# Kernel optimization log

Hardware: AMD Instinct MI355X
Metric: run time of the kernel (lower is better)

The kernel has to match this reference:

```python
import jax, jax.numpy as jnp
import numpy as np

GRID = 32          # grid_size -> N = 1024 patches
NPT = 1            # num_prefix_tokens
SCALE = 8.0        # sqrt(dim_head=64)
EPS = 1e-5         # nn.LayerNorm default eps


def _ln(x, g, b):
    m = jnp.mean(x, axis=-1, keepdims=True)
    v = jnp.var(x, axis=-1, keepdims=True)
    return (x - m) / jnp.sqrt(v + EPS) * g + b


def setup_inputs() -> dict:
    key = jax.random.key(0)
    ks = jax.random.split(key, 12)
    B, T, D, Dh = 32, GRID * GRID + NPT, 768, 64
    s = 0.02
    return {
        "x": jax.random.normal(ks[0], (B, T, D), jnp.float32),
        "Wq": jax.random.normal(ks[1], (D, Dh), jnp.float32) * s,
        "Wk": jax.random.normal(ks[2], (D, Dh), jnp.float32) * s,
        "Wv": jax.random.normal(ks[3], (D, Dh), jnp.float32) * s,
        "gq": jnp.ones((Dh,), jnp.float32),
        "bq": jnp.zeros((Dh,), jnp.float32),
        "gk": jnp.ones((Dh,), jnp.float32),
        "bk": jnp.zeros((Dh,), jnp.float32),
        "Wsig": jax.random.normal(ks[4], (Dh, 2), jnp.float32) * s,
        "bsig": jnp.zeros((2,), jnp.float32),
        "Wa": jax.random.normal(ks[5], (Dh, 1), jnp.float32) * s,
        "ba": jnp.zeros((1,), jnp.float32),
    }


def reference(x, Wq, Wk, Wv, gq, bq, gk, bk, Wsig, bsig, Wa, ba):
    # x: [B, T, D] with T = GRID^2 + NPT
    q = _ln(x @ Wq, gq, bq)            # [B, T, Dh]
    k = _ln(x @ Wk, gk, bk)            # [B, T, Dh]
    v = x @ Wv                          # [B, T, Dh]

    q_patch = q[:, NPT:, :]             # [B, N, Dh]
    alpha = jax.nn.softplus(q_patch @ Wa + ba)[..., 0]   # [B, N]
    sig = jax.nn.sigmoid(q_patch @ Wsig + bsig)          # [B, N, 2]
    sx, sy = sig[..., 0], sig[..., 1]                     # [B, N] each

    # patch-grid relative displacements (vectorized replacement of the
    # O(N^2) python double loop)
    ii, jj = jnp.meshgrid(jnp.arange(GRID), jnp.arange(GRID), indexing="ij")
    coords = jnp.stack([ii.ravel(), jj.ravel()], axis=-1).astype(jnp.float32)  # [N,2]=(y,x)
    dy = coords[:, None, 0] - coords[None, :, 0]          # [N, N]
    dx = coords[:, None, 1] - coords[None, :, 1]          # [N, N]

    # Gaussian bias: G[b,p,q] = exp(-dx^2/(2 sx[b,p]^2) - dy^2/(2 sy[b,p]^2))
    G = jnp.exp(-(dx * dx) / (2.0 * sx[:, :, None] ** 2)
                - (dy * dy) / (2.0 * sy[:, :, None] ** 2))  # [B, N, N]
    S = alpha[:, :, None] * G                               # [B, N, N]

    sim = jnp.einsum("bqd,bkd->bqk", q, k)                  # [B, T, T]
    sim = sim.at[:, NPT:, NPT:].add(S)

    probs = jax.nn.softmax(sim / SCALE, axis=-1)
    return probs @ v                                         # [B, T, Dh]
```

## Files before the change

kernel.cpp:

```cpp
#include <hip/hip_runtime.h>
#include <hip/hip_bf16.h>
#include <math.h>

#define BDIM 32
#define TDIM 1025
#define DDIM 768
#define GRIDW 32
#define TPATCH 1024
#define SCALE 8.0f
#define EPSLN 1e-5f
#define NROW (BDIM * TDIM)
#define VTLD 1088
#define LDP  72
#define LDQ  40
#define NTILES 17

typedef __attribute__((ext_vector_type(8))) short short8v;
typedef __attribute__((ext_vector_type(4))) float f32x4;

__device__ __forceinline__ unsigned short f2bf(float f) {
    unsigned int u = __float_as_uint(f);
    u += 0x7FFFu + ((u >> 16) & 1u);
    return (unsigned short)(u >> 16);
}

__device__ __forceinline__ short8v pack8(float4 a, float4 b) {
    union { short8v v; unsigned short s[8]; } u;
    u.s[0] = f2bf(a.x); u.s[1] = f2bf(a.y); u.s[2] = f2bf(a.z); u.s[3] = f2bf(a.w);
    u.s[4] = f2bf(b.x); u.s[5] = f2bf(b.y); u.s[6] = f2bf(b.z); u.s[7] = f2bf(b.w);
    return u.v;
}

__device__ __forceinline__ void wg_barrier() {
    asm volatile("s_waitcnt lgkmcnt(0)" ::: "memory");
    __builtin_amdgcn_s_barrier();
    __builtin_amdgcn_sched_barrier(0);
}

template<int CTRL>
__device__ __forceinline__ float dpp_f(float x) {
    return __int_as_float(__builtin_amdgcn_update_dpp(
        __float_as_int(x), __float_as_int(x), CTRL, 0xF, 0xF, true));
}
__device__ __forceinline__ float red16_max(float x) {
    x = fmaxf(x, dpp_f<0xB1>(x));
    x = fmaxf(x, dpp_f<0x4E>(x));
    x = fmaxf(x, dpp_f<0x124>(x));
    x = fmaxf(x, dpp_f<0x128>(x));
    return x;
}
__device__ __forceinline__ float red16_sum(float x) {
    x += dpp_f<0xB1>(x);
    x += dpp_f<0x4E>(x);
    x += dpp_f<0x124>(x);
    x += dpp_f<0x128>(x);
    return x;
}

__global__ __launch_bounds__(256) void prep_w_kernel(
    const float* __restrict__ Wq, const float* __restrict__ Wk,
    const float* __restrict__ Wv, unsigned short* __restrict__ wT)
{
    const int c = blockIdx.x;
    const float* W = (c < 64) ? Wq : (c < 128) ? Wk : Wv;
    const int cc = c & 63;
    for (int k = threadIdx.x; k < DDIM; k += 256)
        wT[(size_t)c * DDIM + k] = f2bf(W[(size_t)k * 64 + cc]);
}

__global__ __launch_bounds__(256) void qkv_tile_kernel(
    const float* __restrict__ x, const unsigned short* __restrict__ wT,
    const float* __restrict__ gq, const float* __restrict__ bq,
    const float* __restrict__ gk, const float* __restrict__ bk,
    const float* __restrict__ Wsig, const float* __restrict__ bsig,
    const float* __restrict__ Wa, const float* __restrict__ ba,
    unsigned short* __restrict__ qb, unsigned short* __restrict__ kb,
    unsigned short* __restrict__ vb,
    float* __restrict__ a8, float* __restrict__ isx, float* __restrict__ isy)
{
    __shared__ unsigned short As[2][64][LDQ];
    __shared__ unsigned short Bs[2][192][LDQ];

    const int t  = threadIdx.x;
    const int wv = t >> 6;
    const int ln = t & 63;
    const int lq = ln >> 4;
    const int lr = ln & 15;
    const int tok0 = blockIdx.x * 64;

    const int arow = t >> 2;
    const int aseg = t & 3;
    const float* aptr = x + (size_t)min(tok0 + arow, NROW - 1) * DDIM + aseg * 8;
    const int brow = t >> 2;
    const int bseg = t & 3;

    f32x4 acc[12];
#pragma unroll
    for (int ni = 0; ni < 12; ++ni) acc[ni] = (f32x4){0.f, 0.f, 0.f, 0.f};

    float4 ra0, ra1;
    short8v rb0, rb1, rb2;

    ra0 = *(const float4*)(aptr + 0);
    ra1 = *(const float4*)(aptr + 4);
    rb0 = *(const short8v*)&wT[(size_t)(brow +   0) * DDIM + bseg * 8];
    rb1 = *(const short8v*)&wT[(size_t)(brow +  64) * DDIM + bseg * 8];
    rb2 = *(const short8v*)&wT[(size_t)(brow + 128) * DDIM + bseg * 8];

#pragma unroll
    for (int ks = 0; ks < 24; ++ks) {
        const int buf = ks & 1;
        *(short8v*)&As[buf][arow][aseg * 8]        = pack8(ra0, ra1);
        *(short8v*)&Bs[buf][brow +   0][bseg * 8]  = rb0;
        *(short8v*)&Bs[buf][brow +  64][bseg * 8]  = rb1;
        *(short8v*)&Bs[buf][brow + 128][bseg * 8]  = rb2;
        if (ks + 1 < 24) {
            const int k0 = (ks + 1) * 32;
            ra0 = *(const float4*)(aptr + k0 + 0);
            ra1 = *(const float4*)(aptr + k0 + 4);
            rb0 = *(const short8v*)&wT[(size_t)(brow +   0) * DDIM + k0 + bseg * 8];
            rb1 = *(const short8v*)&wT[(size_t)(brow +  64) * DDIM + k0 + bseg * 8];
            rb2 = *(const short8v*)&wT[(size_t)(brow + 128) * DDIM + k0 + bseg * 8];
        }
        __syncthreads();
        short8v af = *(const short8v*)&As[buf][wv * 16 + lr][lq * 8];
#pragma unroll
        for (int ni = 0; ni < 12; ++ni) {
            short8v bf = *(const short8v*)&Bs[buf][16 * ni + lr][lq * 8];
            acc[ni] = __builtin_amdgcn_mfma_f32_16x16x32_bf16(af, bf, acc[ni], 0, 0, 0);
        }
    }

    float gqv[4], bqv[4], gkv[4], bkv[4], wav[4], ws0[4], ws1[4];
#pragma unroll
    for (int ni = 0; ni < 4; ++ni) {
        int c = lr + 16 * ni;
        gqv[ni] = gq[c]; bqv[ni] = bq[c];
        gkv[ni] = gk[c]; bkv[ni] = bk[c];
        wav[ni] = Wa[c];
        ws0[ni] = Wsig[2 * c];
        ws1[ni] = Wsig[2 * c + 1];
    }
    const float ba0 = ba[0], bs0 = bsig[0], bs1 = bsig[1];

#pragma unroll
    for (int reg = 0; reg < 4; ++reg) {
        const int tokr = tok0 + wv * 16 + lq * 4 + reg;

        float s1 = 0.f, s2 = 0.f;
#pragma unroll
        for (int ni = 0; ni < 4; ++ni) {
            float v = acc[ni][reg];
            s1 += v; s2 += v * v;
        }
#pragma unroll
        for (int off = 1; off < 16; off <<= 1) {
            s1 += __shfl_xor(s1, off);
            s2 += __shfl_xor(s2, off);
        }
        float mean = s1 * (1.f / 64.f);
        float var  = s2 * (1.f / 64.f) - mean * mean;
        float rstd = rsqrtf(var + EPSLN);
        float qn[4];
#pragma unroll
        for (int ni = 0; ni < 4; ++ni)
            qn[ni] = (acc[ni][reg] - mean) * rstd * gqv[ni] + bqv[ni];

        s1 = 0.f; s2 = 0.f;
#pragma unroll
        for (int ni = 0; ni < 4; ++ni) {
            float v = acc[4 + ni][reg];
            s1 += v; s2 += v * v;
        }
#pragma unroll
        for (int off = 1; off < 16; off <<= 1) {
            s1 += __shfl_xor(s1, off);
            s2 += __shfl_xor(s2, off);
        }
        mean = s1 * (1.f / 64.f);
        var  = s2 * (1.f / 64.f) - mean * mean;
        rstd = rsqrtf(var + EPSLN);
        float kn[4];
#pragma unroll
        for (int ni = 0; ni < 4; ++ni)
            kn[ni] = (acc[4 + ni][reg] - mean) * rstd * gkv[ni] + bkv[ni];

        float da = 0.f, d0 = 0.f, d1 = 0.f;
#pragma unroll
        for (int ni = 0; ni < 4; ++ni) {
            da += qn[ni] * wav[ni];
            d0 += qn[ni] * ws0[ni];
            d1 += qn[ni] * ws1[ni];
        }
#pragma unroll
        for (int off = 1; off < 16; off <<= 1) {
            da += __shfl_xor(da, off);
            d0 += __shfl_xor(d0, off);
            d1 += __shfl_xor(d1, off);
        }

        if (tokr < NROW) {
            size_t base = (size_t)tokr * 64;
            int bidx = tokr / TDIM;
            int ti   = tokr - bidx * TDIM;
#pragma unroll
            for (int ni = 0; ni < 4; ++ni) {
                int c = lr + 16 * ni;
                qb[base + c] = f2bf(qn[ni]);
                kb[base + c] = f2bf(kn[ni]);
                vb[base + c] = f2bf(acc[8 + ni][reg]);
            }
            if (lr == 0 && ti >= 1) {
                int p = bidx * TPATCH + ti - 1;
                float av = da + ba0;
                float sp = (av > 20.f) ? av : log1pf(__expf(av));
                a8[p] = sp * (1.f / SCALE);
                float sx = 1.f / (1.f + __expf(-(d0 + bs0)));
                float sy = 1.f / (1.f + __expf(-(d1 + bs1)));
                isx[p] = 0.5f / (sx * sx);
                isy[p] = 0.5f / (sy * sy);
            }
        }
    }
}

__global__ __launch_bounds__(256) void vtrans_kernel(
    const unsigned short* __restrict__ vb, unsigned short* __restrict__ vT)
{
    __shared__ unsigned short tile[64][LDP];
    const int t  = threadIdx.x;
    const int bb = blockIdx.y;
    const int t0 = blockIdx.x * 64;

#pragma unroll
    for (int it = 0; it < 2; ++it) {
        int lin = t + it * 256;
        int tok = lin >> 3;
        int d0  = (lin & 7) * 8;
        short8v v8 = {0, 0, 0, 0, 0, 0, 0, 0};
        if (t0 + tok < TDIM)
            v8 = *(const short8v*)&vb[((size_t)bb * TDIM + t0 + tok) * 64 + d0];
        union { short8v v; unsigned short s[8]; } u; u.v = v8;
#pragma unroll
        for (int j = 0; j < 8; ++j) tile[d0 + j][tok] = u.s[j];
    }
    __syncthreads();

    const int dh = t >> 2;
    const int ch = t & 3;
    short8v o0 = *(const short8v*)&tile[dh][ch * 16];
    short8v o1 = *(const short8v*)&tile[dh][ch * 16 + 8];
    size_t dst = ((size_t)bb * 64 + dh) * VTLD + t0 + ch * 16;
    *(short8v*)&vT[dst]     = o0;
    *(short8v*)&vT[dst + 8] = o1;
}

__global__ __launch_bounds__(256) void attn_mfma_kernel(
    const unsigned short* __restrict__ qb, const unsigned short* __restrict__ kb,
    const unsigned short* __restrict__ vT,
    const float* __restrict__ a8, const float* __restrict__ isx,
    const float* __restrict__ isy, float* __restrict__ out)
{
    __shared__ unsigned short Ks[2][64][LDP];
    __shared__ unsigned short Vt[2][64][LDP];
    __shared__ unsigned short Pt[4][16][LDP];

    const int t  = threadIdx.x;
    const int wv = t >> 6;
    const int ln = t & 63;
    const int lq = ln >> 4;
    const int lr = ln & 15;
    const int bb = blockIdx.y;
    const int q0 = blockIdx.x * 64;

    const int qrow = min(q0 + wv * 16 + lr, TDIM - 1);
    const size_t qbase = ((size_t)bb * TDIM + qrow) * 64;
    const short8v aq0 = *(const short8v*)&qb[qbase + lq * 8];
    const short8v aq1 = *(const short8v*)&qb[qbase + 32 + lq * 8];

    float a8q[4], sxq[4], syq[4], qpy[4], qpx[4];
    bool  hasS[4];
#pragma unroll
    for (int reg = 0; reg < 4; ++reg) {
        int qg = q0 + wv * 16 + lq * 4 + reg;
        hasS[reg] = false;
        a8q[reg] = 0.f; sxq[reg] = 0.f; syq[reg] = 0.f; qpy[reg] = 0.f; qpx[reg] = 0.f;
        if (qg >= 1 && qg < TDIM) {
            int qp = qg - 1;
            hasS[reg] = true;
            a8q[reg] = a8 [bb * TPATCH + qp];
            sxq[reg] = isx[bb * TPATCH + qp];
            syq[reg] = isy[bb * TPATCH + qp];
            qpy[reg] = (float)(qp >> 5);
            qpx[reg] = (float)(qp & 31);
        }
    }

    float m[4]  = {-1e30f, -1e30f, -1e30f, -1e30f};
    float l[4]  = {0.f, 0.f, 0.f, 0.f};
    f32x4 oacc[4];
#pragma unroll
    for (int ni = 0; ni < 4; ++ni) oacc[ni] = (f32x4){0.f, 0.f, 0.f, 0.f};

    const int sk_row = t >> 3;
    const int sk_d0  = (t & 7) * 8;
    short8v rk[2], rv[2];

#define ALOAD(KT0)                                                             \
    do {                                                                       \
        _Pragma("unroll") for (int it = 0; it < 2; ++it) {                     \
            int key = sk_row + 32 * it;                                        \
            int kg  = (KT0) + key;                                             \
            rk[it] = (kg < TDIM)                                               \
                ? *(const short8v*)&kb[((size_t)bb * TDIM + kg) * 64 + sk_d0]  \
                : (short8v){0, 0, 0, 0, 0, 0, 0, 0};                           \
            rv[it] = *(const short8v*)&vT[((size_t)bb * 64 + key) * VTLD +     \
                                          (KT0) + sk_d0];                      \
        }                                                                      \
    } while (0)

#define ASTORE(BUF)                                                            \
    do {                                                                       \
        _Pragma("unroll") for (int it = 0; it < 2; ++it) {                     \
            *(short8v*)&Ks[BUF][sk_row + 32 * it][sk_d0] = rk[it];             \
            *(short8v*)&Vt[BUF][sk_row + 32 * it][sk_d0] = rv[it];             \
        }                                                                      \
    } while (0)

    ALOAD(0);
    ASTORE(0);
    wg_barrier();

    for (int tile = 0; tile < NTILES; ++tile) {
        const int kt0 = tile * 64;
        const int buf = tile & 1;
        if (tile + 1 < NTILES) ALOAD(kt0 + 64);

        f32x4 sac[4];
#pragma unroll
        for (int ni = 0; ni < 4; ++ni) sac[ni] = (f32x4){0.f, 0.f, 0.f, 0.f};
#pragma unroll
        for (int ni = 0; ni < 4; ++ni) {
            short8v b0 = *(const short8v*)&Ks[buf][16 * ni + lr][lq * 8];
            short8v b1 = *(const short8v*)&Ks[buf][16 * ni + lr][32 + lq * 8];
            sac[ni] = __builtin_amdgcn_mfma_f32_16x16x32_bf16(aq0, b0, sac[ni], 0, 0, 0);
            sac[ni] = __builtin_amdgcn_mfma_f32_16x16x32_bf16(aq1, b1, sac[ni], 0, 0, 0);
        }

#pragma unroll
        for (int ni = 0; ni < 4; ++ni) {
            int key = kt0 + 16 * ni + lr;
            int kp  = key - 1;
            float ky = (float)(kp >> 5);
            float kx = (float)(kp & 31);
            bool kvalid = (key >= 1) && (key < TDIM);
#pragma unroll
            for (int reg = 0; reg < 4; ++reg) {
                float z = sac[ni][reg] * (1.f / SCALE);
                if (kvalid && hasS[reg]) {
                    float dy = qpy[reg] - ky;
                    float dx = qpx[reg] - kx;
                    z += a8q[reg] * __expf(-(dx * dx * sxq[reg] + dy * dy * syq[reg]));
                }
                if (key >= TDIM) z = -1e30f;
                sac[ni][reg] = z;
            }
        }

        float scf[4];
#pragma unroll
        for (int reg = 0; reg < 4; ++reg) {
            float mx = fmaxf(fmaxf(sac[0][reg], sac[1][reg]),
                             fmaxf(sac[2][reg], sac[3][reg]));
            mx = red16_max(mx);
            float mn = fmaxf(m[reg], mx);
            scf[reg] = __expf(m[reg] - mn);
            m[reg] = mn;
            float ts = 0.f;
#pragma unroll
            for (int ni = 0; ni < 4; ++ni) {
                float pp = __expf(sac[ni][reg] - mn);
                sac[ni][reg] = pp;
                ts += pp;
            }
            ts = red16_sum(ts);
            l[reg] = l[reg] * scf[reg] + ts;
        }
#pragma unroll
        for (int ni = 0; ni < 4; ++ni)
#pragma unroll
            for (int reg = 0; reg < 4; ++reg)
                oacc[ni][reg] *= scf[reg];

#pragma unroll
        for (int ni = 0; ni < 4; ++ni)
#pragma unroll
            for (int reg = 0; reg < 4; ++reg)
                Pt[wv][lq * 4 + reg][16 * ni + lr] = f2bf(sac[ni][reg]);

#pragma unroll
        for (int ks = 0; ks < 2; ++ks) {
            short8v pa = *(const short8v*)&Pt[wv][lr][ks * 32 + lq * 8];
#pragma unroll
            for (int ni = 0; ni < 4; ++ni) {
                short8v bv = *(const short8v*)&Vt[buf][16 * ni + lr][ks * 32 + lq * 8];
                oacc[ni] = __builtin_amdgcn_mfma_f32_16x16x32_bf16(pa, bv, oacc[ni], 0, 0, 0);
            }
        }

        if (tile + 1 < NTILES) ASTORE(buf ^ 1);
        wg_barrier();
    }
#undef ALOAD
#undef ASTORE

#pragma unroll
    for (int reg = 0; reg < 4; ++reg) {
        int qg = q0 + wv * 16 + lq * 4 + reg;
        if (qg < TDIM) {
            float rl = 1.f / l[reg];
#pragma unroll
            for (int ni = 0; ni < 4; ++ni)
                out[((size_t)bb * TDIM + qg) * 64 + 16 * ni + lr] = oacc[ni][reg] * rl;
        }
    }
}

extern "C" void kernel_launch(void* const* d_in, const int* in_sizes, int n_in,
                              void* d_out, int out_size, void* d_ws, size_t ws_size,
                              hipStream_t stream)
{
    const float* x    = (const float*)d_in[0];
    const float* Wq   = (const float*)d_in[1];
    const float* Wk   = (const float*)d_in[2];
    const float* Wv   = (const float*)d_in[3];
    const float* gq   = (const float*)d_in[4];
    const float* bq   = (const float*)d_in[5];
    const float* gk   = (const float*)d_in[6];
    const float* bk   = (const float*)d_in[7];
    const float* Wsig = (const float*)d_in[8];
    const float* bsig = (const float*)d_in[9];
    const float* Wa   = (const float*)d_in[10];
    const float* ba   = (const float*)d_in[11];
    float* out = (float*)d_out;

    char* w = (char*)d_ws;
    const size_t NQ = (size_t)NROW * 64;
    unsigned short* qb = (unsigned short*)w;   w += NQ * 2;
    unsigned short* kb = (unsigned short*)w;   w += NQ * 2;
    unsigned short* vb = (unsigned short*)w;   w += NQ * 2;
    unsigned short* vT = (unsigned short*)w;   w += (size_t)BDIM * 64 * VTLD * 2;
    float* a8  = (float*)w;                    w += (size_t)BDIM * TPATCH * 4;
    float* isx = (float*)w;                    w += (size_t)BDIM * TPATCH * 4;
    float* isy = (float*)w;                    w += (size_t)BDIM * TPATCH * 4;
    unsigned short* wT = (unsigned short*)w;   w += (size_t)192 * DDIM * 2;

    hipLaunchKernelGGL(prep_w_kernel, dim3(192), dim3(256), 0, stream,
                       Wq, Wk, Wv, wT);

    const int nblk1 = (NROW + 63) / 64;
    hipLaunchKernelGGL(qkv_tile_kernel, dim3(nblk1), dim3(256), 0, stream,
                       x, wT, gq, bq, gk, bk, Wsig, bsig, Wa, ba,
                       qb, kb, vb, a8, isx, isy);

    hipLaunchKernelGGL(vtrans_kernel, dim3(17, BDIM), dim3(256), 0, stream,
                       vb, vT);

    hipLaunchKernelGGL(attn_mfma_kernel, dim3(17, BDIM), dim3(256), 0, stream,
                       qb, kb, vT, a8, isx, isy, out);
}
```

Measured before the change: 95.28 us.

## Stage QKV projection tiles with direct global-to-LDS loads and swizzled layout

The QKV projection kernel now loads x and the pre-tiled bf16 weights straight into LDS using global_load_lds, with an XOR swizzle on the fp32 x tile. The fp32 to bf16 conversion moves to the point where fragments are read from LDS. Block size drops to 128 threads covering 32 tokens, and the weights are reordered per k-step so each stage is one contiguous copy. The aim is to cut register staging and VGPR round trips, but it doubles weight traffic per token and halves per-block work. The epilogue still indexes tokens with wv*16+lq*4, and with only 2 waves that may not match the old code.

```diff
diff --git a/kernel.cpp b/kernel.cpp
--- a/kernel.cpp
+++ b/kernel.cpp
@@ -12,7 +12,6 @@
 #define NROW (BDIM * TDIM)
 #define VTLD 1088
 #define LDP  72
-#define LDQ  40
 #define NTILES 17
 
 typedef __attribute__((ext_vector_type(8))) short short8v;
@@ -30,6 +29,11 @@
     u.s[4] = f2bf(b.x); u.s[5] = f2bf(b.y); u.s[6] = f2bf(b.z); u.s[7] = f2bf(b.w);
     return u.v;
 }
+
+#define GLOAD16(g, l)                                                          \
+    __builtin_amdgcn_global_load_lds(                                          \
+        (const __attribute__((address_space(1))) void*)(g),                    \
+        (__attribute__((address_space(3))) void*)(l), 16, 0, 0)
 
 __device__ __forceinline__ void wg_barrier() {
     asm volatile("s_waitcnt lgkmcnt(0)" ::: "memory");
@@ -59,17 +63,19 @@
 
 __global__ __launch_bounds__(256) void prep_w_kernel(
     const float* __restrict__ Wq, const float* __restrict__ Wk,
-    const float* __restrict__ Wv, unsigned short* __restrict__ wT)
+    const float* __restrict__ Wv, unsigned short* __restrict__ wTt)
 {
     const int c = blockIdx.x;
     const float* W = (c < 64) ? Wq : (c < 128) ? Wk : Wv;
     const int cc = c & 63;
-    for (int k = threadIdx.x; k < DDIM; k += 256)
-        wT[(size_t)c * DDIM + k] = f2bf(W[(size_t)k * 64 + cc]);
-}
-
-__global__ __launch_bounds__(256) void qkv_tile_kernel(
-    const float* __restrict__ x, const unsigned short* __restrict__ wT,
+    for (int k = threadIdx.x; k < DDIM; k += 256) {
+        int ks = k >> 5, kk = k & 31;
+        wTt[(size_t)ks * 6144 + c * 32 + kk] = f2bf(W[(size_t)k * 64 + cc]);
+    }
+}
+
+__global__ __launch_bounds__(128) void qkv_tile_kernel(
+    const float* __restrict__ x, const unsigned short* __restrict__ wTt,
     const float* __restrict__ gq, const float* __restrict__ bq,
     const float* __restrict__ gk, const float* __restrict__ bk,
     const float* __restrict__ Wsig, const float* __restrict__ bsig,
@@ -78,58 +84,72 @@
     unsigned short* __restrict__ vb,
     float* __restrict__ a8, float* __restrict__ isx, float* __restrict__ isy)
 {
-    __shared__ unsigned short As[2][64][LDQ];
-    __shared__ unsigned short Bs[2][192][LDQ];
+    __shared__ float          As[2][32][32];
+    __shared__ unsigned short Bs[2][192][32];
 
     const int t  = threadIdx.x;
     const int wv = t >> 6;
     const int ln = t & 63;
     const int lq = ln >> 4;
     const int lr = ln & 15;
-    const int tok0 = blockIdx.x * 64;
-
-    const int arow = t >> 2;
-    const int aseg = t & 3;
-    const float* aptr = x + (size_t)min(tok0 + arow, NROW - 1) * DDIM + aseg * 8;
-    const int brow = t >> 2;
-    const int bseg = t & 3;
+    const int tok0 = blockIdx.x * 32;
+
+    const char* xB = (const char*)x;
+
+#define STAGE(BUF, KS)                                                         \
+    do {                                                                       \
+        const char* wB = (const char*)wTt + (size_t)(KS) * 12288;              \
+        if (wv == 0) {                                                         \
+            _Pragma("unroll") for (int c = 0; c < 4; ++c) {                    \
+                int L = c * 1024 + ln * 16;                                    \
+                int row = L >> 7;                                              \
+                int seg = ((L >> 4) & 7) ^ (row & 7);                          \
+                const char* g = xB + (size_t)(tok0 + row) * 3072 +             \
+                                (size_t)(KS) * 128 + seg * 16;                 \
+                GLOAD16(g, (char*)&As[BUF][0][0] + c * 1024);                  \
+            }                                                                  \
+            _Pragma("unroll") for (int c = 0; c < 4; ++c)                      \
+                GLOAD16(wB + c * 1024 + ln * 16,                               \
+                        (char*)&Bs[BUF][0][0] + c * 1024);                     \
+        } else {                                                               \
+            _Pragma("unroll") for (int c = 4; c < 12; ++c)                     \
+                GLOAD16(wB + c * 1024 + ln * 16,                               \
+                        (char*)&Bs[BUF][0][0] + c * 1024);                     \
+        }                                                                      \
+    } while (0)
+
+#define COMPUTE(BUF)                                                           \
+    do {                                                                       \
+        const int arow = wv * 16 + lr;                                         \
+        const int x7 = arow & 7;                                               \
+        const char* ab = (const char*)&As[BUF][arow][0];                       \
+        float4 f0 = *(const float4*)(ab + (((lq * 2)     ^ x7) * 16));         \
+        float4 f1 = *(const float4*)(ab + (((lq * 2 + 1) ^ x7) * 16));         \
+        short8v af = pack8(f0, f1);                                            \
+        _Pragma("unroll") for (int ni = 0; ni < 12; ++ni) {                    \
+            short8v bf = *(const short8v*)&Bs[BUF][16 * ni + lr][lq * 8];      \
+            acc[ni] = __builtin_amdgcn_mfma_f32_16x16x32_bf16(af, bf,          \
+                                                              acc[ni], 0, 0, 0); \
+        }                                                                      \
+    } while (0)
 
     f32x4 acc[12];
 #pragma unroll
     for (int ni = 0; ni < 12; ++ni) acc[ni] = (f32x4){0.f, 0.f, 0.f, 0.f};
 
-    float4 ra0, ra1;
-    short8v rb0, rb1, rb2;
-
-    ra0 = *(const float4*)(aptr + 0);
-    ra1 = *(const float4*)(aptr + 4);
-    rb0 = *(const short8v*)&wT[(size_t)(brow +   0) * DDIM + bseg * 8];
-    rb1 = *(const short8v*)&wT[(size_t)(brow +  64) * DDIM + bseg * 8];
-    rb2 = *(const short8v*)&wT[(size_t)(brow + 128) * DDIM + bseg * 8];
-
-#pragma unroll
-    for (int ks = 0; ks < 24; ++ks) {
-        const int buf = ks & 1;
-        *(short8v*)&As[buf][arow][aseg * 8]        = pack8(ra0, ra1);
-        *(short8v*)&Bs[buf][brow +   0][bseg * 8]  = rb0;
-        *(short8v*)&Bs[buf][brow +  64][bseg * 8]  = rb1;
-        *(short8v*)&Bs[buf][brow + 128][bseg * 8]  = rb2;
-        if (ks + 1 < 24) {
-            const int k0 = (ks + 1) * 32;
-            ra0 = *(const float4*)(aptr + k0 + 0);
-            ra1 = *(const float4*)(aptr + k0 + 4);
-            rb0 = *(const short8v*)&wT[(size_t)(brow +   0) * DDIM + k0 + bseg * 8];
-            rb1 = *(const short8v*)&wT[(size_t)(brow +  64) * DDIM + k0 + bseg * 8];
-            rb2 = *(const short8v*)&wT[(size_t)(brow + 128) * DDIM + k0 + bseg * 8];
-        }
+    STAGE(0, 0);
+    __syncthreads();
+
+    for (int ks = 0; ks < 24; ks += 2) {
+        if (ks + 1 < 24) STAGE(1, ks + 1);
+        COMPUTE(0);
         __syncthreads();
-        short8v af = *(const short8v*)&As[buf][wv * 16 + lr][lq * 8];
-#pragma unroll
-        for (int ni = 0; ni < 12; ++ni) {
-            short8v bf = *(const short8v*)&Bs[buf][16 * ni + lr][lq * 8];
-            acc[ni] = __builtin_amdgcn_mfma_f32_16x16x32_bf16(af, bf, acc[ni], 0, 0, 0);
-        }
-    }
+        if (ks + 2 < 24) STAGE(0, ks + 2);
+        COMPUTE(1);
+        __syncthreads();
+    }
+#undef STAGE
+#undef COMPUTE
 
     float gqv[4], bqv[4], gkv[4], bkv[4], wav[4], ws0[4], ws1[4];
 #pragma unroll
@@ -453,14 +473,14 @@
     float* a8  = (float*)w;                    w += (size_t)BDIM * TPATCH * 4;
     float* isx = (float*)w;                    w += (size_t)BDIM * TPATCH * 4;
     float* isy = (float*)w;                    w += (size_t)BDIM * TPATCH * 4;
-    unsigned short* wT = (unsigned short*)w;   w += (size_t)192 * DDIM * 2;
+    unsigned short* wTt = (unsigned short*)w;  w += (size_t)192 * DDIM * 2;
 
     hipLaunchKernelGGL(prep_w_kernel, dim3(192), dim3(256), 0, stream,
-                       Wq, Wk, Wv, wT);
-
-    const int nblk1 = (NROW + 63) / 64;
-    hipLaunchKernelGGL(qkv_tile_kernel, dim3(nblk1), dim3(256), 0, stream,
-                       x, wT, gq, bq, gk, bk, Wsig, bsig, Wa, ba,
+                       Wq, Wk, Wv, wTt);
+
+    const int nblk1 = NROW / 32;
+    hipLaunchKernelGGL(qkv_tile_kernel, dim3(nblk1), dim3(128), 0, stream,
+                       x, wTt, gq, bq, gk, bk, Wsig, bsig, Wa, ba,
                        qb, kb, vb, a8, isx, isy);
 
     hipLaunchKernelGGL(vtrans_kernel, dim3(17, BDIM), dim3(256), 0, stream,
```

New measurement: 99.99 us. 1.05x slower.

## Restructure QKV projection: 32-token tiles, full-row A staging, split-N warps

Applied to the files above, without the earlier changes.

The QKV projection kernel now processes 32 tokens per block instead of 64, which doubles the grid. Each block loads its full 32x768 slice of x into shared memory up front with coalesced float4 loads and bf16 conversion. The four warps are split into 2 row halves by 2 column halves, so each warp accumulates 6 MFMA tiles instead of 12, and only the weight tiles stay double-buffered, using a retiled weight layout that gives contiguous loads. This aims to improve occupancy and global load coalescing, at the cost of a large shared-memory A buffer and LayerNorm work split across warp roles.

```diff
diff --git a/kernel.cpp b/kernel.cpp
--- a/kernel.cpp
+++ b/kernel.cpp
@@ -12,7 +12,8 @@
 #define NROW (BDIM * TDIM)
 #define VTLD 1088
 #define LDP  72
-#define LDQ  40
+#define LDA  772
+#define LDB  40
 #define NTILES 17
 
 typedef __attribute__((ext_vector_type(8))) short short8v;
@@ -22,13 +23,6 @@
     unsigned int u = __float_as_uint(f);
     u += 0x7FFFu + ((u >> 16) & 1u);
     return (unsigned short)(u >> 16);
-}
-
-__device__ __forceinline__ short8v pack8(float4 a, float4 b) {
-    union { short8v v; unsigned short s[8]; } u;
-    u.s[0] = f2bf(a.x); u.s[1] = f2bf(a.y); u.s[2] = f2bf(a.z); u.s[3] = f2bf(a.w);
-    u.s[4] = f2bf(b.x); u.s[5] = f2bf(b.y); u.s[6] = f2bf(b.z); u.s[7] = f2bf(b.w);
-    return u.v;
 }
 
 __device__ __forceinline__ void wg_barrier() {
@@ -59,17 +53,19 @@
 
 __global__ __launch_bounds__(256) void prep_w_kernel(
     const float* __restrict__ Wq, const float* __restrict__ Wk,
-    const float* __restrict__ Wv, unsigned short* __restrict__ wT)
+    const float* __restrict__ Wv, unsigned short* __restrict__ wTt)
 {
     const int c = blockIdx.x;
     const float* W = (c < 64) ? Wq : (c < 128) ? Wk : Wv;
     const int cc = c & 63;
-    for (int k = threadIdx.x; k < DDIM; k += 256)
-        wT[(size_t)c * DDIM + k] = f2bf(W[(size_t)k * 64 + cc]);
+    for (int k = threadIdx.x; k < DDIM; k += 256) {
+        int ks = k >> 5, kk = k & 31;
+        wTt[(size_t)ks * 6144 + c * 32 + kk] = f2bf(W[(size_t)k * 64 + cc]);
+    }
 }
 
 __global__ __launch_bounds__(256) void qkv_tile_kernel(
-    const float* __restrict__ x, const unsigned short* __restrict__ wT,
+    const float* __restrict__ x, const unsigned short* __restrict__ wTt,
     const float* __restrict__ gq, const float* __restrict__ bq,
     const float* __restrict__ gk, const float* __restrict__ bk,
     const float* __restrict__ Wsig, const float* __restrict__ bsig,
@@ -78,74 +74,101 @@
     unsigned short* __restrict__ vb,
     float* __restrict__ a8, float* __restrict__ isx, float* __restrict__ isy)
 {
-    __shared__ unsigned short As[2][64][LDQ];
-    __shared__ unsigned short Bs[2][192][LDQ];
+    __shared__ unsigned short As[32][LDA];
+    __shared__ unsigned short Bs[2][192][LDB];
 
     const int t  = threadIdx.x;
     const int wv = t >> 6;
+    const int rh = wv & 1;
+    const int nh = wv >> 1;
     const int ln = t & 63;
     const int lq = ln >> 4;
     const int lr = ln & 15;
-    const int tok0 = blockIdx.x * 64;
-
-    const int arow = t >> 2;
-    const int aseg = t & 3;
-    const float* aptr = x + (size_t)min(tok0 + arow, NROW - 1) * DDIM + aseg * 8;
-    const int brow = t >> 2;
-    const int bseg = t & 3;
-
-    f32x4 acc[12];
-#pragma unroll
-    for (int ni = 0; ni < 12; ++ni) acc[ni] = (f32x4){0.f, 0.f, 0.f, 0.f};
-
-    float4 ra0, ra1;
-    short8v rb0, rb1, rb2;
-
-    ra0 = *(const float4*)(aptr + 0);
-    ra1 = *(const float4*)(aptr + 4);
-    rb0 = *(const short8v*)&wT[(size_t)(brow +   0) * DDIM + bseg * 8];
-    rb1 = *(const short8v*)&wT[(size_t)(brow +  64) * DDIM + bseg * 8];
-    rb2 = *(const short8v*)&wT[(size_t)(brow + 128) * DDIM + bseg * 8];
-
-#pragma unroll
+    const int tok0 = blockIdx.x * 32;
+
+    {
+        const float4* xsp = (const float4*)(x + (size_t)tok0 * DDIM);
+        float4 ga[6], gb[6];
+#define ALOADG(R, G)                                                           \
+        _Pragma("unroll") for (int j = 0; j < 6; ++j)                          \
+            R[j] = xsp[t + 256 * ((G) * 6 + j)];
+#define APROCG(R, G)                                                           \
+        _Pragma("unroll") for (int j = 0; j < 6; ++j) {                        \
+            int f0 = (t + 256 * ((G) * 6 + j)) * 4;                            \
+            int row = f0 / DDIM;                                               \
+            int col = f0 - row * DDIM;                                         \
+            ushort4 pk;                                                        \
+            pk.x = f2bf(R[j].x); pk.y = f2bf(R[j].y);                          \
+            pk.z = f2bf(R[j].z); pk.w = f2bf(R[j].w);                          \
+            *(ushort4*)&As[row][col] = pk;                                     \
+        }
+        ALOADG(ga, 0);
+        ALOADG(gb, 1);
+        APROCG(ga, 0);
+        ALOADG(ga, 2);
+        APROCG(gb, 1);
+        ALOADG(gb, 3);
+        APROCG(ga, 2);
+        APROCG(gb, 3);
+#undef ALOADG
+#undef APROCG
+    }
+
+    short8v rb[3];
+#define BLOAD(KS)                                                              \
+    _Pragma("unroll") for (int j = 0; j < 3; ++j)                              \
+        rb[j] = *(const short8v*)&wTt[(size_t)(KS) * 6144 +                    \
+                                      (size_t)(t + 256 * j) * 8];
+#define BSTORE(BUF)                                                            \
+    _Pragma("unroll") for (int j = 0; j < 3; ++j) {                            \
+        int idx = t + 256 * j;                                                 \
+        *(short8v*)&Bs[BUF][idx >> 2][(idx & 3) * 8] = rb[j];                  \
+    }
+
+    f32x4 acc[6];
+#pragma unroll
+    for (int j = 0; j < 6; ++j) acc[j] = (f32x4){0.f, 0.f, 0.f, 0.f};
+
+    BLOAD(0);
+    BSTORE(0);
+    __syncthreads();
+
+    const int arow = rh * 16 + lr;
     for (int ks = 0; ks < 24; ++ks) {
         const int buf = ks & 1;
-        *(short8v*)&As[buf][arow][aseg * 8]        = pack8(ra0, ra1);
-        *(short8v*)&Bs[buf][brow +   0][bseg * 8]  = rb0;
-        *(short8v*)&Bs[buf][brow +  64][bseg * 8]  = rb1;
-        *(short8v*)&Bs[buf][brow + 128][bseg * 8]  = rb2;
-        if (ks + 1 < 24) {
-            const int k0 = (ks + 1) * 32;
-            ra0 = *(const float4*)(aptr + k0 + 0);
-            ra1 = *(const float4*)(aptr + k0 + 4);
-            rb0 = *(const short8v*)&wT[(size_t)(brow +   0) * DDIM + k0 + bseg * 8];
-            rb1 = *(const short8v*)&wT[(size_t)(brow +  64) * DDIM + k0 + bseg * 8];
-            rb2 = *(const short8v*)&wT[(size_t)(brow + 128) * DDIM + k0 + bseg * 8];
-        }
+        if (ks + 1 < 24) BLOAD(ks + 1);
+        short8v af = *(const short8v*)&As[arow][ks * 32 + lq * 8];
+#pragma unroll
+        for (int j = 0; j < 6; ++j) {
+            int frag = (j < 4) ? (nh * 4 + j) : (8 + nh * 2 + (j - 4));
+            short8v bf = *(const short8v*)&Bs[buf][16 * frag + lr][lq * 8];
+            acc[j] = __builtin_amdgcn_mfma_f32_16x16x32_bf16(af, bf, acc[j], 0, 0, 0);
+        }
+        if (ks + 1 < 24) BSTORE(buf ^ 1);
         __syncthreads();
-        short8v af = *(const short8v*)&As[buf][wv * 16 + lr][lq * 8];
-#pragma unroll
-        for (int ni = 0; ni < 12; ++ni) {
-            short8v bf = *(const short8v*)&Bs[buf][16 * ni + lr][lq * 8];
-            acc[ni] = __builtin_amdgcn_mfma_f32_16x16x32_bf16(af, bf, acc[ni], 0, 0, 0);
-        }
-    }
-
-    float gqv[4], bqv[4], gkv[4], bkv[4], wav[4], ws0[4], ws1[4];
+    }
+#undef BLOAD
+#undef BSTORE
+
+    float gv[4], bv[4], wav[4], ws0[4], ws1[4];
 #pragma unroll
     for (int ni = 0; ni < 4; ++ni) {
         int c = lr + 16 * ni;
-        gqv[ni] = gq[c]; bqv[ni] = bq[c];
-        gkv[ni] = gk[c]; bkv[ni] = bk[c];
-        wav[ni] = Wa[c];
-        ws0[ni] = Wsig[2 * c];
-        ws1[ni] = Wsig[2 * c + 1];
+        if (nh == 0) {
+            gv[ni] = gq[c]; bv[ni] = bq[c];
+            wav[ni] = Wa[c];
+            ws0[ni] = Wsig[2 * c];
+            ws1[ni] = Wsig[2 * c + 1];
+        } else {
+            gv[ni] = gk[c]; bv[ni] = bk[c];
+            wav[ni] = 0.f; ws0[ni] = 0.f; ws1[ni] = 0.f;
+        }
     }
     const float ba0 = ba[0], bs0 = bsig[0], bs1 = bsig[1];
 
 #pragma unroll
     for (int reg = 0; reg < 4; ++reg) {
-        const int tokr = tok0 + wv * 16 + lq * 4 + reg;
+        const int tokr = tok0 + rh * 16 + lq * 4 + reg;
 
         float s1 = 0.f, s2 = 0.f;
 #pragma unroll
@@ -161,64 +184,46 @@
         float mean = s1 * (1.f / 64.f);
         float var  = s2 * (1.f / 64.f) - mean * mean;
         float rstd = rsqrtf(var + EPSLN);
-        float qn[4];
+        float xn[4];
 #pragma unroll
         for (int ni = 0; ni < 4; ++ni)
-            qn[ni] = (acc[ni][reg] - mean) * rstd * gqv[ni] + bqv[ni];
-
-        s1 = 0.f; s2 = 0.f;
-#pragma unroll
-        for (int ni = 0; ni < 4; ++ni) {
-            float v = acc[4 + ni][reg];
-            s1 += v; s2 += v * v;
-        }
-#pragma unroll
-        for (int off = 1; off < 16; off <<= 1) {
-            s1 += __shfl_xor(s1, off);
-            s2 += __shfl_xor(s2, off);
-        }
-        mean = s1 * (1.f / 64.f);
-        var  = s2 * (1.f / 64.f) - mean * mean;
-        rstd = rsqrtf(var + EPSLN);
-        float kn[4];
+            xn[ni] = (acc[ni][reg] - mean) * rstd * gv[ni] + bv[ni];
+
+        size_t base = (size_t)tokr * 64;
+        unsigned short* dst = (nh == 0) ? qb : kb;
 #pragma unroll
         for (int ni = 0; ni < 4; ++ni)
-            kn[ni] = (acc[4 + ni][reg] - mean) * rstd * gkv[ni] + bkv[ni];
-
-        float da = 0.f, d0 = 0.f, d1 = 0.f;
-#pragma unroll
-        for (int ni = 0; ni < 4; ++ni) {
-            da += qn[ni] * wav[ni];
-            d0 += qn[ni] * ws0[ni];
-            d1 += qn[ni] * ws1[ni];
-        }
-#pragma unroll
-        for (int off = 1; off < 16; off <<= 1) {
-            da += __shfl_xor(da, off);
-            d0 += __shfl_xor(d0, off);
-            d1 += __shfl_xor(d1, off);
-        }
-
-        if (tokr < NROW) {
-            size_t base = (size_t)tokr * 64;
-            int bidx = tokr / TDIM;
-            int ti   = tokr - bidx * TDIM;
+            dst[base + lr + 16 * ni] = f2bf(xn[ni]);
+        vb[base + lr + 32 * nh]      = f2bf(acc[4][reg]);
+        vb[base + lr + 32 * nh + 16] = f2bf(acc[5][reg]);
+
+        if (nh == 0) {
+            float da = 0.f, d0 = 0.f, d1 = 0.f;
 #pragma unroll
             for (int ni = 0; ni < 4; ++ni) {
-                int c = lr + 16 * ni;
-                qb[base + c] = f2bf(qn[ni]);
-                kb[base + c] = f2bf(kn[ni]);
-                vb[base + c] = f2bf(acc[8 + ni][reg]);
-            }
-            if (lr == 0 && ti >= 1) {
-                int p = bidx * TPATCH + ti - 1;
-                float av = da + ba0;
-                float sp = (av > 20.f) ? av : log1pf(__expf(av));
-                a8[p] = sp * (1.f / SCALE);
-                float sx = 1.f / (1.f + __expf(-(d0 + bs0)));
-                float sy = 1.f / (1.f + __expf(-(d1 + bs1)));
-                isx[p] = 0.5f / (sx * sx);
-                isy[p] = 0.5f / (sy * sy);
+                da += xn[ni] * wav[ni];
+                d0 += xn[ni] * ws0[ni];
+                d1 += xn[ni] * ws1[ni];
+            }
+#pragma unroll
+            for (int off = 1; off < 16; off <<= 1) {
+                da += __shfl_xor(da, off);
+                d0 += __shfl_xor(d0, off);
+                d1 += __shfl_xor(d1, off);
+            }
+            if (lr == 0) {
+                int bidx = tokr / TDIM;
+                int ti   = tokr - bidx * TDIM;
+                if (ti >= 1) {
+                    int p = bidx * TPATCH + ti - 1;
+                    float av = da + ba0;
+                    float sp = (av > 20.f) ? av : log1pf(__expf(av));
+                    a8[p] = sp * (1.f / SCALE);
+                    float sx = 1.f / (1.f + __expf(-(d0 + bs0)));
+                    float sy = 1.f / (1.f + __expf(-(d1 + bs1)));
+                    isx[p] = 0.5f / (sx * sx);
+                    isy[p] = 0.5f / (sy * sy);
+                }
             }
         }
     }
@@ -453,14 +458,14 @@
     float* a8  = (float*)w;                    w += (size_t)BDIM * TPATCH * 4;
     float* isx = (float*)w;                    w += (size_t)BDIM * TPATCH * 4;
     float* isy = (float*)w;                    w += (size_t)BDIM * TPATCH * 4;
-    unsigned short* wT = (unsigned short*)w;   w += (size_t)192 * DDIM * 2;
+    unsigned short* wTt = (unsigned short*)w;  w += (size_t)192 * DDIM * 2;
 
     hipLaunchKernelGGL(prep_w_kernel, dim3(192), dim3(256), 0, stream,
-                       Wq, Wk, Wv, wT);
-
-    const int nblk1 = (NROW + 63) / 64;
+                       Wq, Wk, Wv, wTt);
+
+    const int nblk1 = NROW / 32;
     hipLaunchKernelGGL(qkv_tile_kernel, dim3(nblk1), dim3(256), 0, stream,
-                       x, wT, gq, bq, gk, bk, Wsig, bsig, Wa, ba,
+                       x, wTt, gq, bq, gk, bk, Wsig, bsig, Wa, ba,
                        qb, kb, vb, a8, isx, isy);
 
     hipLaunchKernelGGL(vtrans_kernel, dim3(17, BDIM), dim3(256), 0, stream,
```

Result: slower. 124.1 us (+30.2%).

## Double query rows per wave in attention kernel to reuse K/V tiles

Applied to the files above, without the earlier changes.

Each wave now handles 32 query rows (two 16-row MFMA tiles) instead of 16, so each block covers 128 queries and K/V tiles loaded into shared memory are reused twice as much. The grid is swapped so batch is the fast dimension, and s_setprio is raised around the MFMA sections. The aim is to halve K/V global and LDS traffic per query. In exchange, register pressure roughly doubles, and the grid shrinks to 288 blocks, which may underfill the 256 CUs and leave a partial second wave.

```diff
diff --git a/kernel.cpp b/kernel.cpp
--- a/kernel.cpp
+++ b/kernel.cpp
@@ -14,6 +14,7 @@
 #define LDP  72
 #define LDQ  40
 #define NTILES 17
+#define NQT   9
 
 typedef __attribute__((ext_vector_type(8))) short short8v;
 typedef __attribute__((ext_vector_type(4))) float f32x4;
@@ -229,8 +230,8 @@
 {
     __shared__ unsigned short tile[64][LDP];
     const int t  = threadIdx.x;
-    const int bb = blockIdx.y;
-    const int t0 = blockIdx.x * 64;
+    const int bb = blockIdx.x;
+    const int t0 = blockIdx.y * 64;
 
 #pragma unroll
     for (int it = 0; it < 2; ++it) {
@@ -263,44 +264,56 @@
 {
     __shared__ unsigned short Ks[2][64][LDP];
     __shared__ unsigned short Vt[2][64][LDP];
-    __shared__ unsigned short Pt[4][16][LDP];
+    __shared__ unsigned short Pt[4][32][LDP];
 
     const int t  = threadIdx.x;
     const int wv = t >> 6;
     const int ln = t & 63;
     const int lq = ln >> 4;
     const int lr = ln & 15;
-    const int bb = blockIdx.y;
-    const int q0 = blockIdx.x * 64;
-
-    const int qrow = min(q0 + wv * 16 + lr, TDIM - 1);
-    const size_t qbase = ((size_t)bb * TDIM + qrow) * 64;
-    const short8v aq0 = *(const short8v*)&qb[qbase + lq * 8];
-    const short8v aq1 = *(const short8v*)&qb[qbase + 32 + lq * 8];
-
-    float a8q[4], sxq[4], syq[4], qpy[4], qpx[4];
-    bool  hasS[4];
+    const int bb = blockIdx.x;
+    const int q0 = blockIdx.y * 128;
+
+    short8v aq[2][2];
+#pragma unroll
+    for (int mi = 0; mi < 2; ++mi) {
+        int qrow = min(q0 + wv * 32 + mi * 16 + lr, TDIM - 1);
+        size_t qbase = ((size_t)bb * TDIM + qrow) * 64;
+        aq[mi][0] = *(const short8v*)&qb[qbase + lq * 8];
+        aq[mi][1] = *(const short8v*)&qb[qbase + 32 + lq * 8];
+    }
+
+    float a8q[2][4], sxq[2][4], syq[2][4], qpy[2][4], qpx[2][4];
+    bool  hasS[2][4];
+#pragma unroll
+    for (int mi = 0; mi < 2; ++mi)
 #pragma unroll
     for (int reg = 0; reg < 4; ++reg) {
-        int qg = q0 + wv * 16 + lq * 4 + reg;
-        hasS[reg] = false;
-        a8q[reg] = 0.f; sxq[reg] = 0.f; syq[reg] = 0.f; qpy[reg] = 0.f; qpx[reg] = 0.f;
+        int qg = q0 + wv * 32 + mi * 16 + lq * 4 + reg;
+        hasS[mi][reg] = false;
+        a8q[mi][reg] = 0.f; sxq[mi][reg] = 0.f; syq[mi][reg] = 0.f;
+        qpy[mi][reg] = 0.f; qpx[mi][reg] = 0.f;
         if (qg >= 1 && qg < TDIM) {
             int qp = qg - 1;
-            hasS[reg] = true;
-            a8q[reg] = a8 [bb * TPATCH + qp];
-            sxq[reg] = isx[bb * TPATCH + qp];
-            syq[reg] = isy[bb * TPATCH + qp];
-            qpy[reg] = (float)(qp >> 5);
-            qpx[reg] = (float)(qp & 31);
-        }
-    }
-
-    float m[4]  = {-1e30f, -1e30f, -1e30f, -1e30f};
-    float l[4]  = {0.f, 0.f, 0.f, 0.f};
-    f32x4 oacc[4];
-#pragma unroll
-    for (int ni = 0; ni < 4; ++ni) oacc[ni] = (f32x4){0.f, 0.f, 0.f, 0.f};
+            hasS[mi][reg] = true;
+            a8q[mi][reg] = a8 [bb * TPATCH + qp];
+            sxq[mi][reg] = isx[bb * TPATCH + qp];
+            syq[mi][reg] = isy[bb * TPATCH + qp];
+            qpy[mi][reg] = (float)(qp >> 5);
+            qpx[mi][reg] = (float)(qp & 31);
+        }
+    }
+
+    float m[2][4], l[2][4];
+    f32x4 oacc[2][4];
+#pragma unroll
+    for (int mi = 0; mi < 2; ++mi)
+#pragma unroll
+    for (int ni = 0; ni < 4; ++ni) {
+        oacc[mi][ni] = (f32x4){0.f, 0.f, 0.f, 0.f};
+        m[mi][ni] = -1e30f;
+        l[mi][ni] = 0.f;
+    }
 
     const int sk_row = t >> 3;
     const int sk_d0  = (t & 7) * 8;
@@ -336,16 +349,23 @@
         const int buf = tile & 1;
         if (tile + 1 < NTILES) ALOAD(kt0 + 64);
 
-        f32x4 sac[4];
-#pragma unroll
-        for (int ni = 0; ni < 4; ++ni) sac[ni] = (f32x4){0.f, 0.f, 0.f, 0.f};
+        f32x4 sac[2][4];
+#pragma unroll
+        for (int mi = 0; mi < 2; ++mi)
+#pragma unroll
+        for (int ni = 0; ni < 4; ++ni) sac[mi][ni] = (f32x4){0.f, 0.f, 0.f, 0.f};
+        __builtin_amdgcn_s_setprio(1);
 #pragma unroll
         for (int ni = 0; ni < 4; ++ni) {
             short8v b0 = *(const short8v*)&Ks[buf][16 * ni + lr][lq * 8];
             short8v b1 = *(const short8v*)&Ks[buf][16 * ni + lr][32 + lq * 8];
-            sac[ni] = __builtin_amdgcn_mfma_f32_16x16x32_bf16(aq0, b0, sac[ni], 0, 0, 0);
-            sac[ni] = __builtin_amdgcn_mfma_f32_16x16x32_bf16(aq1, b1, sac[ni], 0, 0, 0);
-        }
+#pragma unroll
+            for (int mi = 0; mi < 2; ++mi) {
+                sac[mi][ni] = __builtin_amdgcn_mfma_f32_16x16x32_bf16(aq[mi][0], b0, sac[mi][ni], 0, 0, 0);
+                sac[mi][ni] = __builtin_amdgcn_mfma_f32_16x16x32_bf16(aq[mi][1], b1, sac[mi][ni], 0, 0, 0);
+            }
+        }
+        __builtin_amdgcn_s_setprio(0);
 
 #pragma unroll
         for (int ni = 0; ni < 4; ++ni) {
@@ -355,58 +375,71 @@
             float kx = (float)(kp & 31);
             bool kvalid = (key >= 1) && (key < TDIM);
 #pragma unroll
+            for (int mi = 0; mi < 2; ++mi)
+#pragma unroll
             for (int reg = 0; reg < 4; ++reg) {
-                float z = sac[ni][reg] * (1.f / SCALE);
-                if (kvalid && hasS[reg]) {
-                    float dy = qpy[reg] - ky;
-                    float dx = qpx[reg] - kx;
-                    z += a8q[reg] * __expf(-(dx * dx * sxq[reg] + dy * dy * syq[reg]));
+                float z = sac[mi][ni][reg] * (1.f / SCALE);
+                if (kvalid && hasS[mi][reg]) {
+                    float dy = qpy[mi][reg] - ky;
+                    float dx = qpx[mi][reg] - kx;
+                    z += a8q[mi][reg] * __expf(-(dx * dx * sxq[mi][reg] + dy * dy * syq[mi][reg]));
                 }
                 if (key >= TDIM) z = -1e30f;
-                sac[ni][reg] = z;
+                sac[mi][ni][reg] = z;
             }
         }
 
-        float scf[4];
+        float scf[2][4];
+#pragma unroll
+        for (int mi = 0; mi < 2; ++mi)
 #pragma unroll
         for (int reg = 0; reg < 4; ++reg) {
-            float mx = fmaxf(fmaxf(sac[0][reg], sac[1][reg]),
-                             fmaxf(sac[2][reg], sac[3][reg]));
+            float mx = fmaxf(fmaxf(sac[mi][0][reg], sac[mi][1][reg]),
+                             fmaxf(sac[mi][2][reg], sac[mi][3][reg]));
             mx = red16_max(mx);
-            float mn = fmaxf(m[reg], mx);
-            scf[reg] = __expf(m[reg] - mn);
-            m[reg] = mn;
+            float mn = fmaxf(m[mi][reg], mx);
+            scf[mi][reg] = __expf(m[mi][reg] - mn);
+            m[mi][reg] = mn;
             float ts = 0.f;
 #pragma unroll
             for (int ni = 0; ni < 4; ++ni) {
-                float pp = __expf(sac[ni][reg] - mn);
-                sac[ni][reg] = pp;
+                float pp = __expf(sac[mi][ni][reg] - mn);
+                sac[mi][ni][reg] = pp;
                 ts += pp;
             }
             ts = red16_sum(ts);
-            l[reg] = l[reg] * scf[reg] + ts;
-        }
+            l[mi][reg] = l[mi][reg] * scf[mi][reg] + ts;
+        }
+#pragma unroll
+        for (int mi = 0; mi < 2; ++mi)
 #pragma unroll
         for (int ni = 0; ni < 4; ++ni)
 #pragma unroll
             for (int reg = 0; reg < 4; ++reg)
-                oacc[ni][reg] *= scf[reg];
-
+                oacc[mi][ni][reg] *= scf[mi][reg];
+
+#pragma unroll
+        for (int mi = 0; mi < 2; ++mi)
 #pragma unroll
         for (int ni = 0; ni < 4; ++ni)
 #pragma unroll
             for (int reg = 0; reg < 4; ++reg)
-                Pt[wv][lq * 4 + reg][16 * ni + lr] = f2bf(sac[ni][reg]);
-
+                Pt[wv][mi * 16 + lq * 4 + reg][16 * ni + lr] = f2bf(sac[mi][ni][reg]);
+
+        __builtin_amdgcn_s_setprio(1);
 #pragma unroll
         for (int ks = 0; ks < 2; ++ks) {
-            short8v pa = *(const short8v*)&Pt[wv][lr][ks * 32 + lq * 8];
-#pragma unroll
-            for (int ni = 0; ni < 4; ++ni) {
-                short8v bv = *(const short8v*)&Vt[buf][16 * ni + lr][ks * 32 + lq * 8];
-                oacc[ni] = __builtin_amdgcn_mfma_f32_16x16x32_bf16(pa, bv, oacc[ni], 0, 0, 0);
+#pragma unroll
+            for (int mi = 0; mi < 2; ++mi) {
+                short8v pa = *(const short8v*)&Pt[wv][mi * 16 + lr][ks * 32 + lq * 8];
+#pragma unroll
+                for (int ni = 0; ni < 4; ++ni) {
+                    short8v bv = *(const short8v*)&Vt[buf][16 * ni + lr][ks * 32 + lq * 8];
+                    oacc[mi][ni] = __builtin_amdgcn_mfma_f32_16x16x32_bf16(pa, bv, oacc[mi][ni], 0, 0, 0);
+                }
             }
         }
+        __builtin_amdgcn_s_setprio(0);
 
         if (tile + 1 < NTILES) ASTORE(buf ^ 1);
         wg_barrier();
@@ -415,13 +448,15 @@
 #undef ASTORE
 
 #pragma unroll
+    for (int mi = 0; mi < 2; ++mi)
+#pragma unroll
     for (int reg = 0; reg < 4; ++reg) {
-        int qg = q0 + wv * 16 + lq * 4 + reg;
+        int qg = q0 + wv * 32 + mi * 16 + lq * 4 + reg;
         if (qg < TDIM) {
-            float rl = 1.f / l[reg];
+            float rl = 1.f / l[mi][reg];
 #pragma unroll
             for (int ni = 0; ni < 4; ++ni)
-                out[((size_t)bb * TDIM + qg) * 64 + 16 * ni + lr] = oacc[ni][reg] * rl;
+                out[((size_t)bb * TDIM + qg) * 64 + 16 * ni + lr] = oacc[mi][ni][reg] * rl;
         }
     }
 }
@@ -463,9 +498,9 @@
                        x, wT, gq, bq, gk, bk, Wsig, bsig, Wa, ba,
                        qb, kb, vb, a8, isx, isy);
 
-    hipLaunchKernelGGL(vtrans_kernel, dim3(17, BDIM), dim3(256), 0, stream,
+    hipLaunchKernelGGL(vtrans_kernel, dim3(BDIM, 17), dim3(256), 0, stream,
                        vb, vT);
 
-    hipLaunchKernelGGL(attn_mfma_kernel, dim3(17, BDIM), dim3(256), 0, stream,
+    hipLaunchKernelGGL(attn_mfma_kernel, dim3(BDIM, NQT), dim3(256), 0, stream,
                        qb, kb, vT, a8, isx, isy, out);
 }
```

New measurement: 106.3 us. 1.12x slower.
